# Kernel optimization log

Hardware: AMD Instinct MI355X
Metric: run time of the kernel (lower is better)

## Reference

```python
import math
import jax, jax.numpy as jnp
import numpy as np

NUM_HEADS = 8


def setup_inputs() -> dict:
    key0 = jax.random.key(0)
    ks = jax.random.split(key0, 11)
    R, C, B, E, Q = 64, 1024, 2, 256, 256
    s = 0.05  # keep pre-softmax scores well-conditioned
    return {
        "query": jax.random.normal(ks[0], (B, Q), jnp.float32),
        "key": jax.random.normal(ks[1], (R, C, B, E), jnp.float32),
        "value": jax.random.normal(ks[2], (R, C, B, E), jnp.float32),
        "Wq": jax.random.normal(ks[3], (E, Q), jnp.float32) * s,
        "bq": jax.random.normal(ks[4], (E,), jnp.float32) * s,
        "Wk": jax.random.normal(ks[5], (E, E), jnp.float32) * s,
        "bk": jax.random.normal(ks[6], (E,), jnp.float32) * s,
        "Wv": jax.random.normal(ks[7], (E, E), jnp.float32) * s,
        "bv": jax.random.normal(ks[8], (E,), jnp.float32) * s,
        "Wo": jax.random.normal(ks[9], (E, E), jnp.float32) * s,
        "bo": jax.random.normal(ks[10], (E,), jnp.float32) * s,
    }


def reference(query, key, value, Wq, bq, Wk, bk, Wv, bv, Wo, bo):
    R, C, B, E = key.shape
    H = NUM_HEADS
    D = E // H
    # main (non-chunked) torch path: align_scaling(query) uses query.size(0) == batch_size
    scaling = (D ** -0.5) / math.sqrt(query.shape[0])
    # projections (torch Linear: x @ W.T + b)
    q = (query @ Wq.T + bq).reshape(B, H, D) * scaling          # [B,H,D]
    k = (key @ Wk.T + bk).reshape(R, C, B, H, D)                # [R,C,B,H,D]
    # tied-row scores: contract over rows r AND head_dim d -> [H,B,C]
    attn_weights = jnp.einsum("nhd,rjnhd->hnj", q, k)
    attn_probs = jax.nn.softmax(attn_weights, axis=-1)          # [H,B,C]
    v = (value @ Wv.T + bv).reshape(R, C, B, H, D)              # [R,C,B,H,D]
    # broadcast probs back per row/column (elementwise scale of v)
    context = jnp.einsum("hnj,rjnhd->rjnhd", attn_probs, v)
    context = context.reshape(R, C, B, E)
    output = context @ Wo.T + bo                                 # [R,C,B,E]
    return output, attn_probs
```

## Files before the change

### kernel.cpp

```cpp
#include <hip/hip_runtime.h>

#define R_DIM 64
#define C_DIM 1024
#define B_DIM 2
#define E_DIM 256
#define Q_DIM 256
#define H_DIM 8
#define D_DIM 32
#define ROW_STRIDE ((size_t)C_DIM * B_DIM * E_DIM)
#define OUT_MAIN ((size_t)R_DIM * C_DIM * B_DIM * E_DIM)

typedef short bf16x8 __attribute__((ext_vector_type(8)));
typedef float f32x4 __attribute__((ext_vector_type(4)));

__device__ __forceinline__ unsigned short f2bf(float x) {
  unsigned int u = __builtin_bit_cast(unsigned int, x);
  u += 0x7FFFu + ((u >> 16) & 1u);
  return (unsigned short)(u >> 16);
}

__global__ void prep_q(const float* __restrict__ query, const float* __restrict__ Wq,
                       const float* __restrict__ bq, float* __restrict__ q_out) {
  int idx = blockIdx.x * 256 + threadIdx.x;
  int n = idx >> 8, e = idx & 255;
  const float4* qr = (const float4*)(query + (size_t)n * Q_DIM);
  const float4* wr = (const float4*)(Wq + (size_t)e * Q_DIM);
  float s = bq[e];
#pragma unroll 8
  for (int k = 0; k < Q_DIM / 4; k++) {
    float4 a = qr[k], b = wr[k];
    s += a.x * b.x + a.y * b.y + a.z * b.z + a.w * b.w;
  }
  q_out[idx] = s * 0.125f;
}

__global__ void prep_w_pack(const float* __restrict__ q, const float* __restrict__ Wk,
                            const float* __restrict__ bk, float* __restrict__ w_out,
                            float* __restrict__ bterm_out,
                            const float* __restrict__ Wv, const float* __restrict__ Wo,
                            unsigned short* __restrict__ B1p, unsigned short* __restrict__ B2p) {
  if (blockIdx.x < 16) {
    int idx = blockIdx.x * 256 + threadIdx.x;
    int e2 = idx & 255;
    int hn = idx >> 8;
    int n = hn & 1, h = hn >> 1;
    float s = 0.f;
#pragma unroll
    for (int d = 0; d < D_DIM; d++)
      s += q[n * E_DIM + h * D_DIM + d] * Wk[(h * D_DIM + d) * E_DIM + e2];
    w_out[idx] = s;
    if (idx < H_DIM * B_DIM) {
      int nn = idx & 1, hh = idx >> 1;
      float sb = 0.f;
#pragma unroll
      for (int d = 0; d < D_DIM; d++)
        sb += q[nn * E_DIM + hh * D_DIM + d] * bk[hh * D_DIM + d];
      bterm_out[idx] = sb;
    }
  } else {
    int gidx = (blockIdx.x - 16) * 256 + threadIdx.x;
    const float* src = (gidx < 8192) ? Wv : Wo;
    unsigned short* dst = (gidx < 8192) ? B1p : B2p;
    int li = gidx & 8191;
    int lane = li & 63;
    int pk = li >> 6;
    int ntile = pk >> 3, kstep = pk & 7;
    int row = ntile * 16 + (lane & 15);
    int col0 = kstep * 32 + (lane >> 4) * 8;
    for (int jj = 0; jj < 8; jj++)
      dst[li * 8 + jj] = f2bf(src[row * E_DIM + col0 + jj]);
  }
}

__global__ void scores_kernel(const float* __restrict__ key, const float* __restrict__ w,
                              const float* __restrict__ bterm, float* __restrict__ scores) {
  const int bid = blockIdx.x;
  const int j = bid >> 1, n = bid & 1;
  const int t = threadIdx.x;
  const int lane = t & 63, wv = t >> 6;

  const float4* kp = (const float4*)(key + ((size_t)j * B_DIM + n) * E_DIM) + lane;
  float4 ks4 = {0.f, 0.f, 0.f, 0.f};
#pragma unroll
  for (int r = wv; r < R_DIM; r += 4) {
    float4 v = kp[(size_t)r * (ROW_STRIDE / 4)];
    ks4.x += v.x; ks4.y += v.y; ks4.z += v.z; ks4.w += v.w;
  }
  __shared__ float red4[4][E_DIM];
  *(float4*)(&red4[wv][lane * 4]) = ks4;
  __syncthreads();
  float ks = red4[0][t] + red4[1][t] + red4[2][t] + red4[3][t];

  __shared__ float red[H_DIM][4];
  for (int h = 0; h < H_DIM; h++) {
    float p = ks * w[(h * B_DIM + n) * E_DIM + t];
    for (int off = 32; off > 0; off >>= 1) p += __shfl_down(p, off, 64);
    if (lane == 0) red[h][wv] = p;
  }
  __syncthreads();
  if (t < H_DIM) {
    float s = red[t][0] + red[t][1] + red[t][2] + red[t][3] +
              (float)R_DIM * bterm[t * B_DIM + n];
    scores[(t * B_DIM + n) * C_DIM + j] = s;
  }
}

__global__ void softmax_kernel(const float* __restrict__ scores, float* __restrict__ probs,
                               float* __restrict__ probs_out) {
  const int hn = blockIdx.x;
  const int t = threadIdx.x;
  const float* s = scores + (size_t)hn * C_DIM;
  float v[4];
  float mx = -1e30f;
  for (int i = 0; i < 4; i++) {
    v[i] = s[t + i * 256];
    mx = fmaxf(mx, v[i]);
  }
  __shared__ float sm[4];
  const int lane = t & 63, wv = t >> 6;
  for (int off = 32; off > 0; off >>= 1) mx = fmaxf(mx, __shfl_down(mx, off, 64));
  if (lane == 0) sm[wv] = mx;
  __syncthreads();
  mx = fmaxf(fmaxf(sm[0], sm[1]), fmaxf(sm[2], sm[3]));
  float sum = 0.f;
  for (int i = 0; i < 4; i++) {
    v[i] = expf(v[i] - mx);
    sum += v[i];
  }
  for (int off = 32; off > 0; off >>= 1) sum += __shfl_down(sum, off, 64);
  __syncthreads();
  if (lane == 0) sm[wv] = sum;
  __syncthreads();
  sum = sm[0] + sm[1] + sm[2] + sm[3];
  float inv = 1.0f / sum;
  for (int i = 0; i < 4; i++) {
    float p = v[i] * inv;
    probs[(size_t)hn * C_DIM + t + i * 256] = p;
    probs_out[(size_t)hn * C_DIM + t + i * 256] = p;
  }
}

__global__ __launch_bounds__(512, 4) void fused_pv(
    const float* __restrict__ value, const unsigned short* __restrict__ B1p,
    const unsigned short* __restrict__ B2p, const float* __restrict__ bv,
    const float* __restrict__ bo, const float* __restrict__ probs,
    float* __restrict__ out) {
  __shared__ unsigned short vt[64 * 256];
  __shared__ unsigned short vs[64 * 256];
  const int bid = blockIdx.x;
  const int j = bid >> 1, n = bid & 1;
  const int t = threadIdx.x;
  const int lane = t & 63;
  const int wv = t >> 6;
  const int l15 = lane & 15;
  const int quad = lane >> 4;
  const int Mbase = (wv >> 1) * 64;
  const int Nbase = (wv & 1) * 32;

  const float* vbase = value + ((size_t)j * B_DIM + n) * E_DIM;
#pragma unroll
  for (int row = wv; row < 64; row += 8) {
    const float4 v4 = *(((const float4*)(vbase + (size_t)row * ROW_STRIDE)) + lane);
    ushort4 u;
    u.x = f2bf(v4.x); u.y = f2bf(v4.y); u.z = f2bf(v4.z); u.w = f2bf(v4.w);
    const int col = (lane * 4 + ((row & 12) << 2)) & 255;
    *(ushort4*)(&vt[row * 256 + col]) = u;
  }

  const int vrow0 = Nbase + l15;
  const int vrow1 = Nbase + 16 + l15;
  const int rot0 = (vrow0 & 12) << 2;
  const int rot1 = (vrow1 & 12) << 2;

  f32x4 acc[4][2];
  const f32x4 zero = {0.f, 0.f, 0.f, 0.f};
#pragma unroll
  for (int mt = 0; mt < 4; mt++)
#pragma unroll
    for (int nt = 0; nt < 2; nt++) acc[mt][nt] = zero;

  __syncthreads();

#pragma unroll
  for (int ks = 0; ks < 8; ks++) {
    bf16x8 a[4], b[2];
#pragma unroll
    for (int mt = 0; mt < 4; mt++)
      a[mt] = ((const bf16x8*)B1p)[((((wv >> 1) * 4 + mt) * 8 + ks) * 64 + lane)];
    b[0] = *(const bf16x8*)(&vt[vrow0 * 256 + ((ks * 32 + quad * 8 + rot0) & 255)]);
    b[1] = *(const bf16x8*)(&vt[vrow1 * 256 + ((ks * 32 + quad * 8 + rot1) & 255)]);
#pragma unroll
    for (int mt = 0; mt < 4; mt++)
#pragma unroll
      for (int nt = 0; nt < 2; nt++)
        acc[mt][nt] = __builtin_amdgcn_mfma_f32_16x16x32_bf16(a[mt], b[nt], acc[mt][nt], 0, 0, 0);
  }

  const float p0 = probs[((size_t)(2 * (wv >> 1)) * B_DIM + n) * C_DIM + j];
  const float p1 = probs[((size_t)(2 * (wv >> 1) + 1) * B_DIM + n) * C_DIM + j];

#pragma unroll
  for (int mt = 0; mt < 4; mt++) {
    const int e0 = Mbase + mt * 16 + quad * 4;
    const float4 bvv = *(const float4*)(&bv[e0]);
    const float p = (mt < 2) ? p0 : p1;
#pragma unroll
    for (int nt = 0; nt < 2; nt++) {
      const int vrow = (nt == 0) ? vrow0 : vrow1;
      const int rot = (nt == 0) ? rot0 : rot1;
      ushort4 u;
      u.x = f2bf((acc[mt][nt][0] + bvv.x) * p);
      u.y = f2bf((acc[mt][nt][1] + bvv.y) * p);
      u.z = f2bf((acc[mt][nt][2] + bvv.z) * p);
      u.w = f2bf((acc[mt][nt][3] + bvv.w) * p);
      *(ushort4*)(&vs[vrow * 256 + ((e0 + rot) & 255)]) = u;
      acc[mt][nt] = zero;
    }
  }
  __syncthreads();

#pragma unroll
  for (int ks = 0; ks < 8; ks++) {
    bf16x8 a[4], b[2];
#pragma unroll
    for (int mt = 0; mt < 4; mt++)
      a[mt] = ((const bf16x8*)B2p)[((((wv >> 1) * 4 + mt) * 8 + ks) * 64 + lane)];
    b[0] = *(const bf16x8*)(&vs[vrow0 * 256 + ((ks * 32 + quad * 8 + rot0) & 255)]);
    b[1] = *(const bf16x8*)(&vs[vrow1 * 256 + ((ks * 32 + quad * 8 + rot1) & 255)]);
#pragma unroll
    for (int mt = 0; mt < 4; mt++)
#pragma unroll
      for (int nt = 0; nt < 2; nt++)
        acc[mt][nt] = __builtin_amdgcn_mfma_f32_16x16x32_bf16(a[mt], b[nt], acc[mt][nt], 0, 0, 0);
  }

  float* obase = out + ((size_t)j * B_DIM + n) * E_DIM;
#pragma unroll
  for (int mt = 0; mt < 4; mt++) {
    const int f0 = Mbase + mt * 16 + quad * 4;
    const float4 bov = *(const float4*)(&bo[f0]);
#pragma unroll
    for (int nt = 0; nt < 2; nt++) {
      const int vrow = (nt == 0) ? vrow0 : vrow1;
      float4 r;
      r.x = acc[mt][nt][0] + bov.x;
      r.y = acc[mt][nt][1] + bov.y;
      r.z = acc[mt][nt][2] + bov.z;
      r.w = acc[mt][nt][3] + bov.w;
      *(float4*)(&obase[(size_t)vrow * ROW_STRIDE + f0]) = r;
    }
  }
}

extern "C" void kernel_launch(void* const* d_in, const int* in_sizes, int n_in,
                              void* d_out, int out_size, void* d_ws, size_t ws_size,
                              hipStream_t stream) {
  const float* query = (const float*)d_in[0];
  const float* key   = (const float*)d_in[1];
  const float* value = (const float*)d_in[2];
  const float* Wq = (const float*)d_in[3];
  const float* bq = (const float*)d_in[4];
  const float* Wk = (const float*)d_in[5];
  const float* bk = (const float*)d_in[6];
  const float* Wv = (const float*)d_in[7];
  const float* bv = (const float*)d_in[8];
  const float* Wo = (const float*)d_in[9];
  const float* bo = (const float*)d_in[10];
  float* out = (float*)d_out;

  float* ws_f = (float*)d_ws;
  float* w_ = ws_f;
  float* bterm_ = ws_f + 4096;
  float* scores_ = ws_f + 4112;
  float* q_ = scores_;
  float* probs_ = ws_f + 20496;
  unsigned short* B1p = (unsigned short*)((char*)d_ws + 147520);
  unsigned short* B2p = (unsigned short*)((char*)d_ws + 147520 + 131072);

  prep_q<<<dim3(2), dim3(256), 0, stream>>>(query, Wq, bq, q_);
  prep_w_pack<<<dim3(80), dim3(256), 0, stream>>>(q_, Wk, bk, w_, bterm_, Wv, Wo, B1p, B2p);
  scores_kernel<<<dim3(C_DIM * B_DIM), dim3(256), 0, stream>>>(key, w_, bterm_, scores_);
  softmax_kernel<<<dim3(H_DIM * B_DIM), dim3(256), 0, stream>>>(scores_, probs_,
                                                                out + OUT_MAIN);
  fused_pv<<<dim3(C_DIM * B_DIM), dim3(512), 0, stream>>>(value, B1p, B2p, bv, bo,
                                                          probs_, out);
}
```

Baseline: 402.6 us.

## Reuse single LDS tile for both GEMM stages and remap waves to feature slices

The fused value/output projection kernel now uses one shared 64x256 bf16 tile for both the converted value block and the intermediate scaled context, instead of two separate tiles. A barrier is added before overwriting it. Each wave now owns a 32-feature slice across all 64 rows, which lets it use a single attention probability and loads fewer weight fragments from global memory. Halving shared memory per block and raising the launch-bounds occupancy hint are meant to fit more blocks per CU to better hide memory latency. The cost is an extra barrier and more LDS fragment reads per wave.

```diff
diff --git a/kernel.cpp b/kernel.cpp
--- a/kernel.cpp
+++ b/kernel.cpp
@@ -140,13 +140,12 @@
   }
 }
 
-__global__ __launch_bounds__(512, 4) void fused_pv(
+__global__ __launch_bounds__(512, 6) void fused_pv(
     const float* __restrict__ value, const unsigned short* __restrict__ B1p,
     const unsigned short* __restrict__ B2p, const float* __restrict__ bv,
     const float* __restrict__ bo, const float* __restrict__ probs,
     float* __restrict__ out) {
-  __shared__ unsigned short vt[64 * 256];
-  __shared__ unsigned short vs[64 * 256];
+  __shared__ unsigned short tile[64 * 256];
   const int bid = blockIdx.x;
   const int j = bid >> 1, n = bid & 1;
   const int t = threadIdx.x;
@@ -154,8 +153,8 @@
   const int wv = t >> 6;
   const int l15 = lane & 15;
   const int quad = lane >> 4;
-  const int Mbase = (wv >> 1) * 64;
-  const int Nbase = (wv & 1) * 32;
+
+  const float p = probs[((size_t)wv * B_DIM + n) * C_DIM + j];
 
   const float* vbase = value + ((size_t)j * B_DIM + n) * E_DIM;
 #pragma unroll
@@ -164,56 +163,52 @@
     ushort4 u;
     u.x = f2bf(v4.x); u.y = f2bf(v4.y); u.z = f2bf(v4.z); u.w = f2bf(v4.w);
     const int col = (lane * 4 + ((row & 12) << 2)) & 255;
-    *(ushort4*)(&vt[row * 256 + col]) = u;
-  }
-
-  const int vrow0 = Nbase + l15;
-  const int vrow1 = Nbase + 16 + l15;
-  const int rot0 = (vrow0 & 12) << 2;
-  const int rot1 = (vrow1 & 12) << 2;
-
-  f32x4 acc[4][2];
+    *(ushort4*)(&tile[row * 256 + col]) = u;
+  }
+
+  const int rot = (l15 & 12) << 2;
+
+  f32x4 acc[2][4];
   const f32x4 zero = {0.f, 0.f, 0.f, 0.f};
 #pragma unroll
-  for (int mt = 0; mt < 4; mt++)
-#pragma unroll
-    for (int nt = 0; nt < 2; nt++) acc[mt][nt] = zero;
+  for (int mt = 0; mt < 2; mt++)
+#pragma unroll
+    for (int nt = 0; nt < 4; nt++) acc[mt][nt] = zero;
 
   __syncthreads();
 
 #pragma unroll
   for (int ks = 0; ks < 8; ks++) {
-    bf16x8 a[4], b[2];
-#pragma unroll
-    for (int mt = 0; mt < 4; mt++)
-      a[mt] = ((const bf16x8*)B1p)[((((wv >> 1) * 4 + mt) * 8 + ks) * 64 + lane)];
-    b[0] = *(const bf16x8*)(&vt[vrow0 * 256 + ((ks * 32 + quad * 8 + rot0) & 255)]);
-    b[1] = *(const bf16x8*)(&vt[vrow1 * 256 + ((ks * 32 + quad * 8 + rot1) & 255)]);
-#pragma unroll
-    for (int mt = 0; mt < 4; mt++)
-#pragma unroll
-      for (int nt = 0; nt < 2; nt++)
+    bf16x8 a[2], b[4];
+#pragma unroll
+    for (int mt = 0; mt < 2; mt++)
+      a[mt] = ((const bf16x8*)B1p)[((wv * 2 + mt) * 8 + ks) * 64 + lane];
+    const int bcol = (ks * 32 + quad * 8 + rot) & 255;
+#pragma unroll
+    for (int nt = 0; nt < 4; nt++)
+      b[nt] = *(const bf16x8*)(&tile[(nt * 16 + l15) * 256 + bcol]);
+#pragma unroll
+    for (int mt = 0; mt < 2; mt++)
+#pragma unroll
+      for (int nt = 0; nt < 4; nt++)
         acc[mt][nt] = __builtin_amdgcn_mfma_f32_16x16x32_bf16(a[mt], b[nt], acc[mt][nt], 0, 0, 0);
   }
 
-  const float p0 = probs[((size_t)(2 * (wv >> 1)) * B_DIM + n) * C_DIM + j];
-  const float p1 = probs[((size_t)(2 * (wv >> 1) + 1) * B_DIM + n) * C_DIM + j];
-
-#pragma unroll
-  for (int mt = 0; mt < 4; mt++) {
-    const int e0 = Mbase + mt * 16 + quad * 4;
+  __syncthreads();
+
+#pragma unroll
+  for (int mt = 0; mt < 2; mt++) {
+    const int e0 = wv * 32 + mt * 16 + quad * 4;
     const float4 bvv = *(const float4*)(&bv[e0]);
-    const float p = (mt < 2) ? p0 : p1;
-#pragma unroll
-    for (int nt = 0; nt < 2; nt++) {
-      const int vrow = (nt == 0) ? vrow0 : vrow1;
-      const int rot = (nt == 0) ? rot0 : rot1;
+#pragma unroll
+    for (int nt = 0; nt < 4; nt++) {
+      const int vrow = nt * 16 + l15;
       ushort4 u;
       u.x = f2bf((acc[mt][nt][0] + bvv.x) * p);
       u.y = f2bf((acc[mt][nt][1] + bvv.y) * p);
       u.z = f2bf((acc[mt][nt][2] + bvv.z) * p);
       u.w = f2bf((acc[mt][nt][3] + bvv.w) * p);
-      *(ushort4*)(&vs[vrow * 256 + ((e0 + rot) & 255)]) = u;
+      *(ushort4*)(&tile[vrow * 256 + ((e0 + rot) & 255)]) = u;
       acc[mt][nt] = zero;
     }
   }
@@ -221,27 +216,29 @@
 
 #pragma unroll
   for (int ks = 0; ks < 8; ks++) {
-    bf16x8 a[4], b[2];
-#pragma unroll
-    for (int mt = 0; mt < 4; mt++)
-      a[mt] = ((const bf16x8*)B2p)[((((wv >> 1) * 4 + mt) * 8 + ks) * 64 + lane)];
-    b[0] = *(const bf16x8*)(&vs[vrow0 * 256 + ((ks * 32 + quad * 8 + rot0) & 255)]);
-    b[1] = *(const bf16x8*)(&vs[vrow1 * 256 + ((ks * 32 + quad * 8 + rot1) & 255)]);
-#pragma unroll
-    for (int mt = 0; mt < 4; mt++)
-#pragma unroll
-      for (int nt = 0; nt < 2; nt++)
+    bf16x8 a[2], b[4];
+#pragma unroll
+    for (int mt = 0; mt < 2; mt++)
+      a[mt] = ((const bf16x8*)B2p)[((wv * 2 + mt) * 8 + ks) * 64 + lane];
+    const int bcol = (ks * 32 + quad * 8 + rot) & 255;
+#pragma unroll
+    for (int nt = 0; nt < 4; nt++)
+      b[nt] = *(const bf16x8*)(&tile[(nt * 16 + l15) * 256 + bcol]);
+#pragma unroll
+    for (int mt = 0; mt < 2; mt++)
+#pragma unroll
+      for (int nt = 0; nt < 4; nt++)
         acc[mt][nt] = __builtin_amdgcn_mfma_f32_16x16x32_bf16(a[mt], b[nt], acc[mt][nt], 0, 0, 0);
   }
 
   float* obase = out + ((size_t)j * B_DIM + n) * E_DIM;
 #pragma unroll
-  for (int mt = 0; mt < 4; mt++) {
-    const int f0 = Mbase + mt * 16 + quad * 4;
+  for (int mt = 0; mt < 2; mt++) {
+    const int f0 = wv * 32 + mt * 16 + quad * 4;
     const float4 bov = *(const float4*)(&bo[f0]);
 #pragma unroll
-    for (int nt = 0; nt < 2; nt++) {
-      const int vrow = (nt == 0) ? vrow0 : vrow1;
+    for (int nt = 0; nt < 4; nt++) {
+      const int vrow = nt * 16 + l15;
       float4 r;
       r.x = acc[mt][nt][0] + bov.x;
       r.y = acc[mt][nt][1] + bov.y;
```

Result: faster. 391.3 us (-2.8%).
